# Optimization experiments

Hardware: AMD Instinct MI355X
Metric: run time of the kernel (lower is better)

Reference implementation:

```python
import jax, jax.numpy as jnp
import numpy as np

N_NODES = 50000
N_EDGES = 800000
N_GRAPHS = 128
F_IN = 128
HID = 64
EDGE_DIM = 16
H1, H2 = 4, 2
NEG_SLOPE = 0.2


def _glorot(key, shape, fan_in):
    return jax.random.normal(key, shape, dtype=jnp.float32) / np.sqrt(fan_in)


def setup_inputs() -> dict:
    key = jax.random.key(0)
    ks = jax.random.split(key, 20)
    x = jax.random.normal(ks[0], (N_NODES, F_IN), dtype=jnp.float32)
    edge_attr = jax.random.normal(ks[1], (N_EDGES, EDGE_DIM), dtype=jnp.float32)
    edge_index = jax.random.randint(ks[2], (2, N_EDGES), 0, N_NODES, dtype=jnp.int32)
    # evenly spread graph ids so every graph is non-empty (sorted)
    batch = (jnp.arange(N_NODES, dtype=jnp.int32) * N_GRAPHS) // N_NODES
    p = {
        'W1': _glorot(ks[3], (F_IN, H1 * HID), F_IN),
        'a_src1': _glorot(ks[4], (H1, HID), HID),
        'a_dst1': _glorot(ks[5], (H1, HID), HID),
        'We1': _glorot(ks[6], (EDGE_DIM, H1 * HID), EDGE_DIM),
        'a_e1': _glorot(ks[7], (H1, HID), HID),
        'b1': jnp.zeros((H1 * HID,), jnp.float32),
        'W2': _glorot(ks[8], (H1 * HID, H2 * HID), H1 * HID),
        'a_src2': _glorot(ks[9], (H2, HID), HID),
        'a_dst2': _glorot(ks[10], (H2, HID), HID),
        'We2': _glorot(ks[11], (EDGE_DIM, H2 * HID), EDGE_DIM),
        'a_e2': _glorot(ks[12], (H2, HID), HID),
        'b2': jnp.zeros((HID,), jnp.float32),
        'Wr': _glorot(ks[13], (HID, 1), HID),
        'br': jnp.zeros((1,), jnp.float32),
    }
    return dict(x=x, edge_attr=edge_attr, edge_index=edge_index, batch=batch, **p)


def _segment_softmax(scores, seg, num_segments):
    # scores: [E, H], softmax grouped by seg (destination node)
    m = jax.ops.segment_max(scores, seg, num_segments)
    m = jnp.where(jnp.isfinite(m), m, 0.0)
    ex = jnp.exp(scores - m[seg])
    s = jax.ops.segment_sum(ex, seg, num_segments)
    return ex / (s[seg] + 1e-16)


def _add_self_loops(edge_index, edge_attr, n):
    # PyG add_self_loops with fill_value='mean': per-dst mean of edge_attr
    src, dst = edge_index[0], edge_index[1]
    cnt = jax.ops.segment_sum(jnp.ones((src.shape[0],), jnp.float32), dst, n)
    loop_attr = jax.ops.segment_sum(edge_attr, dst, n) / jnp.maximum(cnt, 1.0)[:, None]
    loop = jnp.arange(n, dtype=src.dtype)
    return (jnp.concatenate([src, loop]), jnp.concatenate([dst, loop]),
            jnp.concatenate([edge_attr, loop_attr], axis=0))


def _gat_layer(x, e_attr, src, dst, W, a_src, a_dst, We, a_e, b, heads, outc, concat):
    n = x.shape[0]
    xs = (x @ W).reshape(n, heads, outc)                 # [N,H,C]
    s_src = jnp.einsum('nhc,hc->nh', xs, a_src)
    s_dst = jnp.einsum('nhc,hc->nh', xs, a_dst)
    ee = (e_attr @ We).reshape(-1, heads, outc)          # [E,H,C]
    s_e = jnp.einsum('ehc,hc->eh', ee, a_e)
    score = jax.nn.leaky_relu(s_src[src] + s_dst[dst] + s_e, NEG_SLOPE)  # [E,H]
    alpha = _segment_softmax(score, dst, n)
    out = jax.ops.segment_sum(xs[src] * alpha[..., None], dst, n)        # [N,H,C]
    out = out.reshape(n, heads * outc) if concat else out.mean(axis=1)
    return out + b


def reference(x, edge_attr, edge_index, batch,
              W1, a_src1, a_dst1, We1, a_e1, b1,
              W2, a_src2, a_dst2, We2, a_e2, b2, Wr, br):
    n = x.shape[0]
    src, dst, ea = _add_self_loops(edge_index, edge_attr, n)
    h = _gat_layer(x, ea, src, dst, W1, a_src1, a_dst1, We1, a_e1, b1, H1, HID, True)
    h = jax.nn.relu(h)
    h = _gat_layer(h, ea, src, dst, W2, a_src2, a_dst2, We2, a_e2, b2, H2, HID, False)
    g = jax.ops.segment_max(h, batch, N_GRAPHS)          # global max pool [G, HID]
    return g @ Wr + br
```

## Files before the change

### kernel.cpp

```cpp
#include <hip/hip_runtime.h>
#include <hip/hip_bf16.h>
#include <hip/hip_fp16.h>

#define DEVINL __device__ __forceinline__
typedef __hip_bfloat16 bf16;

typedef __attribute__((ext_vector_type(8))) __bf16 bf16x8;
typedef __attribute__((ext_vector_type(4))) float f32x4;

static constexpr int N_NODES  = 50000;
static constexpr int N_EDGES  = 800000;
static constexpr int N_GRAPHS = 128;
static constexpr float NEG_SLOPE = 0.2f;

DEVINL float ldIn(const void* __restrict__ p, size_t i, int isbf) {
    if (isbf) return __bfloat162float(((const bf16*)p)[i]);
    return ((const float*)p)[i];
}

DEVINL unsigned short f2bf(float f) {
    bf16 b = __float2bfloat16(f);
    return *reinterpret_cast<unsigned short*>(&b);
}

DEVINL unsigned f2hbits(float f) {
    __half h = __float2half(f);
    return (unsigned)*reinterpret_cast<unsigned short*>(&h);
}

DEVINL float hbits2f(unsigned bits) {
    unsigned short us = (unsigned short)bits;
    __half h = *reinterpret_cast<__half*>(&us);
    return __half2float(h);
}

DEVINL float lrelu_exp(float sc) {
    sc = sc > 0.f ? sc : NEG_SLOPE * sc;
    return __expf(sc);
}

DEVINL void accw(float w, unsigned wv, float& a0, float& a1) {
    a0 = fmaf(w, __uint_as_float(wv << 16), a0);
    a1 = fmaf(w, __uint_as_float(wv & 0xffff0000u), a1);
}

template<int H>
DEVINL float getse(const uint4& rv, int h) {
    unsigned bits;
    if (H == 4) {
        unsigned w16 = (h & 2) ? rv.z : rv.y;
        bits = (h & 1) ? (w16 >> 16) : (w16 & 0xffffu);
    } else {
        bits = h ? (rv.w >> 16) : (rv.w & 0xffffu);
    }
    return hbits2f(bits);
}

template<int CPL> struct XVT;
template<> struct XVT<8> { using T = uint4; };
template<> struct XVT<4> { using T = uint2; };

__global__ void detect_dtype_kernel(const unsigned short* __restrict__ xu,
                                    int* __restrict__ flag)
{
    int t = threadIdx.x;
    int bad = 0;
    for (int i = t; i < 1024; i += 64) {
        unsigned u = xu[2 * i];
        float v = __uint_as_float(u << 16);
        if (!(fabsf(v) <= 1e4f)) bad = 1;
    }
    unsigned long long m = __ballot(bad);
    if (t == 0) *flag = m ? 0 : 1;
}

__global__ void build_M_kernel(const void* __restrict__ We1, const void* __restrict__ ae1,
                               const void* __restrict__ We2, const void* __restrict__ ae2,
                               const int* __restrict__ flagp,
                               float* __restrict__ M1, float* __restrict__ M2)
{
    const int isbf = *flagp;
    int t = threadIdx.x;
    if (t < 64) {
        int d = t >> 2, h = t & 3;
        float s = 0.f;
        for (int c = 0; c < 64; ++c)
            s += ldIn(We1, d * 256 + h * 64 + c, isbf) * ldIn(ae1, h * 64 + c, isbf);
        M1[d * 4 + h] = s;
    }
    if (t < 32) {
        int d = t >> 1, h = t & 1;
        float s = 0.f;
        for (int c = 0; c < 64; ++c)
            s += ldIn(We2, d * 128 + h * 64 + c, isbf) * ldIn(ae2, h * 64 + c, isbf);
        M2[d * 2 + h] = s;
    }
}

template<int K, int M>
__global__ void build_wfrag_kernel(const void* __restrict__ W, const int* __restrict__ flagp,
                                   bf16* __restrict__ Wfrag)
{
    constexpr int KS = K / 32;
    const int isbf = *flagp;
    int idx = blockIdx.x * 256 + threadIdx.x;
    constexpr int total = (M / 16) * KS * 64 * 8;
    if (idx >= total) return;
    int j    = idx & 7;
    int lane = (idx >> 3) & 63;
    int rem  = idx >> 9;
    int ks   = rem % KS;
    int ct   = rem / KS;
    int k = ks * 32 + (lane >> 4) * 8 + j;
    int n = ct * 16 + (lane & 15);
    Wfrag[idx] = __float2bfloat16(ldIn(W, (size_t)k * M + n, isbf));
}

template<int K, int M, int AMODE, int H>
__global__ __launch_bounds__(256)
void gemm_mfma_kernel(const void* __restrict__ A, const bf16* __restrict__ Wfrag,
                      bf16* __restrict__ C, const int* __restrict__ flagp, int N,
                      const void* __restrict__ a_src, const void* __restrict__ a_dst,
                      float* __restrict__ sA, float* __restrict__ sD)
{
    constexpr int KS = K / 32, CT = M / 16;
    constexpr int LDA = K + 8;
    __shared__ __align__(16) unsigned short Asm[64 * LDA];
    const int isbf = *flagp;
    const int tid  = threadIdx.x;
    const int wave = tid >> 6, lane = tid & 63;
    const int n0 = blockIdx.x * 64;

    for (int i = tid; i < 64 * (K / 8); i += 256) {
        int r  = i / (K / 8);
        int kc = (i % (K / 8)) * 8;
        int n  = n0 + r;
        unsigned short v[8] = {0, 0, 0, 0, 0, 0, 0, 0};
        if (n < N) {
            size_t base = (size_t)n * K + kc;
            if (AMODE == 1 || isbf) {
                *reinterpret_cast<uint4*>(v) =
                    *reinterpret_cast<const uint4*>((const unsigned short*)A + base);
            } else {
                const float* Af = (const float*)A + base;
                float4 f0 = *reinterpret_cast<const float4*>(Af);
                float4 f1 = *reinterpret_cast<const float4*>(Af + 4);
                v[0] = f2bf(f0.x); v[1] = f2bf(f0.y); v[2] = f2bf(f0.z); v[3] = f2bf(f0.w);
                v[4] = f2bf(f1.x); v[5] = f2bf(f1.y); v[6] = f2bf(f1.z); v[7] = f2bf(f1.w);
            }
        }
        *reinterpret_cast<uint4*>(&Asm[r * LDA + kc]) = *reinterpret_cast<uint4*>(v);
    }
    __syncthreads();

    f32x4 acc[CT];
    #pragma unroll
    for (int ct = 0; ct < CT; ++ct) acc[ct] = (f32x4){0.f, 0.f, 0.f, 0.f};

    const int arow  = wave * 16 + (lane & 15);
    const int akoff = (lane >> 4) * 8;
    #pragma unroll
    for (int ks = 0; ks < KS; ++ks) {
        bf16x8 af = *reinterpret_cast<const bf16x8*>(&Asm[arow * LDA + ks * 32 + akoff]);
        #pragma unroll
        for (int ct = 0; ct < CT; ++ct) {
            bf16x8 bfr = *reinterpret_cast<const bf16x8*>(
                &Wfrag[(((size_t)ct * KS + ks) * 64 + lane) * 8]);
            acc[ct] = __builtin_amdgcn_mfma_f32_16x16x32_bf16(af, bfr, acc[ct], 0, 0, 0);
        }
    }

    const int crow0 = n0 + wave * 16 + (lane >> 4) * 4;
    const int ccol  = lane & 15;
    #pragma unroll
    for (int ct = 0; ct < CT; ++ct) {
        #pragma unroll
        for (int r = 0; r < 4; ++r) {
            int row = crow0 + r;
            if (row < N) C[(size_t)row * M + ct * 16 + ccol] = __float2bfloat16(acc[ct][r]);
        }
    }

    float psA[4][H], psD[4][H];
    #pragma unroll
    for (int r = 0; r < 4; ++r)
        #pragma unroll
        for (int hh = 0; hh < H; ++hh) { psA[r][hh] = 0.f; psD[r][hh] = 0.f; }
    #pragma unroll
    for (int ct = 0; ct < CT; ++ct) {
        float as = ldIn(a_src, ct * 16 + ccol, isbf);
        float ad = ldIn(a_dst, ct * 16 + ccol, isbf);
        const int hh = ct >> 2;
        #pragma unroll
        for (int r = 0; r < 4; ++r) {
            psA[r][hh] += acc[ct][r] * as;
            psD[r][hh] += acc[ct][r] * ad;
        }
    }
    #pragma unroll
    for (int m = 1; m < 16; m <<= 1) {
        #pragma unroll
        for (int r = 0; r < 4; ++r)
            #pragma unroll
            for (int hh = 0; hh < H; ++hh) {
                psA[r][hh] += __shfl_xor(psA[r][hh], m);
                psD[r][hh] += __shfl_xor(psD[r][hh], m);
            }
    }
    if (ccol == 0) {
        #pragma unroll
        for (int r = 0; r < 4; ++r) {
            int row = crow0 + r;
            if (row < N) {
                #pragma unroll
                for (int hh = 0; hh < H; ++hh) {
                    sA[(size_t)row * H + hh] = psA[r][hh];
                    sD[(size_t)row * H + hh] = psD[r][hh];
                }
            }
        }
    }
}

__global__ void csr_count_kernel(const int* __restrict__ dst, int* __restrict__ cnt,
                                 int* __restrict__ rank)
{
    int e = blockIdx.x * blockDim.x + threadIdx.x;
    if (e >= N_EDGES) return;
    rank[e] = atomicAdd(&cnt[dst[e]], 1);
}

__global__ __launch_bounds__(256)
void scan_sum_kernel(const int* __restrict__ cnt, int* __restrict__ bsum)
{
    __shared__ int sm[256];
    int i = blockIdx.x * 256 + threadIdx.x;
    sm[threadIdx.x] = (i < N_NODES) ? cnt[i] : 0;
    __syncthreads();
    for (int off = 128; off; off >>= 1) {
        if (threadIdx.x < off) sm[threadIdx.x] += sm[threadIdx.x + off];
        __syncthreads();
    }
    if (threadIdx.x == 0) bsum[blockIdx.x] = sm[0];
}

__global__ __launch_bounds__(256)
void scan_off_kernel(int* __restrict__ bsum, int nb)
{
    __shared__ int sm[256];
    int tid = threadIdx.x;
    int v = (tid < nb) ? bsum[tid] : 0;
    sm[tid] = v;
    __syncthreads();
    for (int off = 1; off < 256; off <<= 1) {
        int t = (tid >= off) ? sm[tid - off] : 0;
        __syncthreads();
        sm[tid] += t;
        __syncthreads();
    }
    if (tid < nb) bsum[tid] = sm[tid] - v;
}

__global__ __launch_bounds__(256)
void scan_final_kernel(const int* __restrict__ cnt, const int* __restrict__ bsum,
                       int* __restrict__ row)
{
    __shared__ int sm[256];
    int i = blockIdx.x * 256 + threadIdx.x;
    int tid = threadIdx.x;
    int v = (i < N_NODES) ? cnt[i] : 0;
    sm[tid] = v;
    __syncthreads();
    for (int off = 1; off < 256; off <<= 1) {
        int t = (tid >= off) ? sm[tid - off] : 0;
        __syncthreads();
        sm[tid] += t;
        __syncthreads();
    }
    int excl = sm[tid] - v + bsum[blockIdx.x];
    if (i < N_NODES) row[i] = excl;
    if (i == N_NODES - 1) row[N_NODES] = excl + v;
}

__global__ void csr_scatter_kernel(const int* __restrict__ srcI, const int* __restrict__ dstI,
                                   const void* __restrict__ eattr, const int* __restrict__ flagp,
                                   const float* __restrict__ M1, const float* __restrict__ M2,
                                   const int* __restrict__ row, const int* __restrict__ rank,
                                   uint4* __restrict__ erec)
{
    const int isbf = *flagp;
    int e = blockIdx.x * blockDim.x + threadIdx.x;
    if (e >= N_EDGES) return;
    float attr[16];
    #pragma unroll
    for (int k = 0; k < 16; ++k) attr[k] = ldIn(eattr, (size_t)e * 16 + k, isbf);
    float4 o1 = {0.f, 0.f, 0.f, 0.f};
    float2 o2 = {0.f, 0.f};
    #pragma unroll
    for (int k = 0; k < 16; ++k) {
        o1.x += attr[k] * M1[k * 4 + 0];
        o1.y += attr[k] * M1[k * 4 + 1];
        o1.z += attr[k] * M1[k * 4 + 2];
        o1.w += attr[k] * M1[k * 4 + 3];
        o2.x += attr[k] * M2[k * 2 + 0];
        o2.y += attr[k] * M2[k * 2 + 1];
    }
    int pos = row[dstI[e]] + rank[e];
    uint4 rec;
    rec.x = (unsigned)srcI[e];
    rec.y = f2hbits(o1.x) | (f2hbits(o1.y) << 16);
    rec.z = f2hbits(o1.z) | (f2hbits(o1.w) << 16);
    rec.w = f2hbits(o2.x) | (f2hbits(o2.y) << 16);
    erec[pos] = rec;
}

template<int H, int LAYER>
__global__ __launch_bounds__(256)
void agg_fused_kernel(const int* __restrict__ row, const uint4* __restrict__ erec,
                      const bf16* __restrict__ xs,
                      const float* __restrict__ sA, const float* __restrict__ sD,
                      const void* __restrict__ bias,
                      const int* __restrict__ flagp, void* __restrict__ out)
{
    constexpr int CPL = (H * 64) / 32;
    using XV = typename XVT<CPL>::T;
    const int isbf = *flagp;
    int dv = (blockIdx.x * 256 + threadIdx.x) >> 6;
    const int d = __builtin_amdgcn_readfirstlane(dv);
    const int lane = threadIdx.x & 63;
    if (d >= N_NODES) return;
    const int sub = lane >> 5;
    const int sl  = lane & 31;
    const int h = (sl * CPL) >> 6;
    const unsigned short* xsu = (const unsigned short*)xs;
    const float sDv = sD[(size_t)d * H + h];
    const float sAd = sA[(size_t)d * H + h];

    float acc[CPL];
    #pragma unroll
    for (int i = 0; i < CPL; ++i) acc[i] = 0.f;
    float den = 0.f, seSum = 0.f;

    const int b = row[d], eend = row[d + 1];
    const int nb8 = (eend - b) & ~7;

    for (int j0 = b; j0 < b + nb8; j0 += 8) {
        uint4 rv[4];
        int   s[4];
        XV    xv[4];
        float sa[4], se[4];
        #pragma unroll
        for (int u = 0; u < 4; ++u) rv[u] = erec[j0 + 2 * u + sub];
        #pragma unroll
        for (int u = 0; u < 4; ++u) s[u] = (int)rv[u].x;
        #pragma unroll
        for (int u = 0; u < 4; ++u)
            xv[u] = *reinterpret_cast<const XV*>(&xsu[(size_t)s[u] * (H * 64) + sl * CPL]);
        #pragma unroll
        for (int u = 0; u < 4; ++u) sa[u] = sA[(size_t)s[u] * H + h];
        #pragma unroll
        for (int u = 0; u < 4; ++u) se[u] = getse<H>(rv[u], h);
        #pragma unroll
        for (int u = 0; u < 4; ++u) {
            float w = lrelu_exp(sa[u] + sDv + se[u]);
            seSum += se[u];
            den += w;
            const unsigned* wv = reinterpret_cast<const unsigned*>(&xv[u]);
            #pragma unroll
            for (int p = 0; p < CPL / 2; ++p) accw(w, wv[p], acc[2 * p], acc[2 * p + 1]);
        }
    }
    for (int j0 = b + nb8; j0 < eend; j0 += 2) {
        int jj = j0 + sub;
        bool valid = jj < eend;
        int jc = valid ? jj : (eend - 1);
        uint4 rv = erec[jc];
        int s = (int)rv.x;
        float se = getse<H>(rv, h);
        float sa = sA[(size_t)s * H + h];
        XV xv = *reinterpret_cast<const XV*>(&xsu[(size_t)s * (H * 64) + sl * CPL]);
        float w = valid ? lrelu_exp(sa + sDv + se) : 0.f;
        seSum += valid ? se : 0.f;
        den += w;
        const unsigned* wv = reinterpret_cast<const unsigned*>(&xv);
        #pragma unroll
        for (int p = 0; p < CPL / 2; ++p) accw(w, wv[p], acc[2 * p], acc[2 * p + 1]);
    }

    #pragma unroll
    for (int i = 0; i < CPL; ++i) acc[i] += __shfl_xor(acc[i], 32);
    den   += __shfl_xor(den, 32);
    seSum += __shfl_xor(seSum, 32);

    {
        const int cntv = eend - b;
        const float seM = seSum / fmaxf((float)cntv, 1.f);
        const float wS = lrelu_exp(sAd + sDv + seM);
        XV xv = *reinterpret_cast<const XV*>(&xsu[(size_t)d * (H * 64) + sl * CPL]);
        den += wS;
        const unsigned* wv = reinterpret_cast<const unsigned*>(&xv);
        #pragma unroll
        for (int p = 0; p < CPL / 2; ++p) accw(wS, wv[p], acc[2 * p], acc[2 * p + 1]);
    }

    const float rden = 1.f / (den + 1e-16f);
    if (LAYER == 1) {
        if (sub == 0) {
            unsigned o[CPL / 2];
            #pragma unroll
            for (int p = 0; p < CPL / 2; ++p) {
                float v0 = acc[2 * p] * rden + ldIn(bias, sl * CPL + 2 * p, isbf);
                float v1 = acc[2 * p + 1] * rden + ldIn(bias, sl * CPL + 2 * p + 1, isbf);
                v0 = v0 > 0.f ? v0 : 0.f;
                v1 = v1 > 0.f ? v1 : 0.f;
                o[p] = (unsigned)f2bf(v0) | ((unsigned)f2bf(v1) << 16);
            }
            *reinterpret_cast<uint4*>(&((unsigned short*)out)[(size_t)d * (H * 64) + sl * CPL]) =
                *reinterpret_cast<uint4*>(o);
        }
    } else {
        float v[CPL], p[CPL];
        #pragma unroll
        for (int i = 0; i < CPL; ++i) {
            v[i] = acc[i] * rden;
            p[i] = __shfl_xor(v[i], 16);
        }
        if (lane < 16) {
            float4 o;
            o.x = 0.5f * (v[0] + p[0]) + ldIn(bias, sl * 4 + 0, isbf);
            o.y = 0.5f * (v[1] + p[1]) + ldIn(bias, sl * 4 + 1, isbf);
            o.z = 0.5f * (v[2] + p[2]) + ldIn(bias, sl * 4 + 2, isbf);
            o.w = 0.5f * (v[3] + p[3]) + ldIn(bias, sl * 4 + 3, isbf);
            *reinterpret_cast<float4*>(&((float*)out)[(size_t)d * 64 + sl * 4]) = o;
        }
    }
}

__global__ __launch_bounds__(256)
void pool_max_kernel(const float* __restrict__ h2, const int* __restrict__ batch,
                     float* __restrict__ g)
{
    int gi = blockIdx.x;
    int lo = 0, hi = N_NODES;
    while (lo < hi) { int mid = (lo + hi) >> 1; if (batch[mid] < gi) lo = mid + 1; else hi = mid; }
    int start = lo;
    lo = start; hi = N_NODES;
    while (lo < hi) { int mid = (lo + hi) >> 1; if (batch[mid] < gi + 1) lo = mid + 1; else hi = mid; }
    int end = lo;
    int c = threadIdx.x & 63, chunk = threadIdx.x >> 6;
    float m = -INFINITY;
    for (int n = start + chunk; n < end; n += 4) m = fmaxf(m, h2[(size_t)n * 64 + c]);
    __shared__ float sm[256];
    sm[threadIdx.x] = m;
    __syncthreads();
    if (threadIdx.x < 64) {
        m = fmaxf(fmaxf(sm[threadIdx.x], sm[threadIdx.x + 64]),
                  fmaxf(sm[threadIdx.x + 128], sm[threadIdx.x + 192]));
        g[gi * 64 + threadIdx.x] = m;
    }
}

__global__ void readout_kernel(const float* __restrict__ g, const void* __restrict__ Wr,
                               const void* __restrict__ br, const int* __restrict__ flagp,
                               void* __restrict__ out)
{
    const int isbf = *flagp;
    int gi = blockIdx.x;
    int lane = threadIdx.x;
    float p = g[gi * 64 + lane] * ldIn(Wr, lane, isbf);
    for (int off = 32; off; off >>= 1) p += __shfl_down(p, off);
    if (lane == 0) {
        float r = p + ldIn(br, 0, isbf);
        if (isbf) ((bf16*)out)[gi] = __float2bfloat16(r);
        else      ((float*)out)[gi] = r;
    }
}

extern "C" void kernel_launch(void* const* d_in, const int* in_sizes, int n_in,
                              void* d_out, int out_size, void* d_ws, size_t ws_size,
                              hipStream_t stream)
{
    const void* x     = d_in[0];
    const void* ea    = d_in[1];
    const int*  eidx  = (const int*)d_in[2];
    const int*  batch = (const int*)d_in[3];
    const void* W1  = d_in[4];
    const void* as1 = d_in[5];
    const void* ad1 = d_in[6];
    const void* We1 = d_in[7];
    const void* ae1 = d_in[8];
    const void* b1  = d_in[9];
    const void* W2  = d_in[10];
    const void* as2 = d_in[11];
    const void* ad2 = d_in[12];
    const void* We2 = d_in[13];
    const void* ae2 = d_in[14];
    const void* b2  = d_in[15];
    const void* Wr  = d_in[16];
    const void* br  = d_in[17];

    const int* srcI = eidx;
    const int* dstI = eidx + N_EDGES;

    float* ws    = (float*)d_ws;
    bf16*  xs    = (bf16*)ws;
    bf16*  h1    = (bf16*)(ws + 6400000);
    float* h2    = ws + 6400000;
    uint4* erec  = (uint4*)(ws + 12800000);
    float* sA1   = ws + 16000000;
    float* sD1   = ws + 16200000;
    float* sA2   = ws + 16400000;
    float* sD2   = ws + 16500000;
    int*   ib    = (int*)(ws + 16600000);
    int*   row    = ib;
    int*   cnt    = ib + 50016;
    int*   bsum   = ib + 100032;
    int*   rank   = ib + 100384;
    float* misc  = ws + 16600000 + 900384;
    int*   flag  = (int*)misc;
    float* M1    = misc + 16;
    float* M2    = misc + 80;
    float* gpool = misc + 112;
    bf16*  wf1   = (bf16*)(misc + 8320);
    bf16*  wf2   = (bf16*)(misc + 8320 + 16384);

    hipMemsetAsync(cnt, 0, N_NODES * sizeof(int), stream);

    detect_dtype_kernel<<<1, 64, 0, stream>>>((const unsigned short*)x, flag);
    build_M_kernel<<<1, 64, 0, stream>>>(We1, ae1, We2, ae2, flag, M1, M2);
    build_wfrag_kernel<128, 256><<<128, 256, 0, stream>>>(W1, flag, wf1);
    build_wfrag_kernel<256, 128><<<128, 256, 0, stream>>>(W2, flag, wf2);

    const int NB = (N_NODES + 255) / 256;
    csr_count_kernel<<<(N_EDGES + 255) / 256, 256, 0, stream>>>(dstI, cnt, rank);
    scan_sum_kernel<<<NB, 256, 0, stream>>>(cnt, bsum);
    scan_off_kernel<<<1, 256, 0, stream>>>(bsum, NB);
    scan_final_kernel<<<NB, 256, 0, stream>>>(cnt, bsum, row);
    csr_scatter_kernel<<<(N_EDGES + 255) / 256, 256, 0, stream>>>(
        srcI, dstI, ea, flag, M1, M2, row, rank, erec);

    const int GB = (N_NODES + 63) / 64;

    gemm_mfma_kernel<128, 256, 0, 4><<<GB, 256, 0, stream>>>(
        x, wf1, xs, flag, N_NODES, as1, ad1, sA1, sD1);
    agg_fused_kernel<4, 1><<<(N_NODES + 3) / 4, 256, 0, stream>>>(
        row, erec, xs, sA1, sD1, b1, flag, h1);

    gemm_mfma_kernel<256, 128, 1, 2><<<GB, 256, 0, stream>>>(
        h1, wf2, xs, flag, N_NODES, as2, ad2, sA2, sD2);
    agg_fused_kernel<2, 2><<<(N_NODES + 3) / 4, 256, 0, stream>>>(
        row, erec, xs, sA2, sD2, b2, flag, h2);

    pool_max_kernel<<<N_GRAPHS, 256, 0, stream>>>(h2, batch, gpool);
    readout_kernel<<<N_GRAPHS, 64, 0, stream>>>(gpool, Wr, br, flag, d_out);
}
```

Before: 423.9 us.

## Process four edges per wave in aggregation and fuse prep and pool/readout kernels

The aggregation kernel now splits each 64-lane wave into four 16-lane groups, each handling a different edge with wider 16-byte gathers per lane, in place of two 32-lane halves. A second xor-shuffle stage combines the partial sums. The three weight-prep kernels are merged into one launch, and max-pool is fused with the readout. The aim is more memory-level parallelism in the gather-bound aggregation and fewer small launches, at the cost of more registers per lane and an extra reduction step.

Result: faster. 411.3 us (-3.0%).

```diff
diff --git a/kernel.cpp b/kernel.cpp
--- a/kernel.cpp
+++ b/kernel.cpp
@@ -56,10 +56,6 @@
     return hbits2f(bits);
 }
 
-template<int CPL> struct XVT;
-template<> struct XVT<8> { using T = uint4; };
-template<> struct XVT<4> { using T = uint2; };
-
 __global__ void detect_dtype_kernel(const unsigned short* __restrict__ xu,
                                     int* __restrict__ flag)
 {
@@ -74,36 +70,11 @@
     if (t == 0) *flag = m ? 0 : 1;
 }
 
-__global__ void build_M_kernel(const void* __restrict__ We1, const void* __restrict__ ae1,
-                               const void* __restrict__ We2, const void* __restrict__ ae2,
-                               const int* __restrict__ flagp,
-                               float* __restrict__ M1, float* __restrict__ M2)
-{
-    const int isbf = *flagp;
-    int t = threadIdx.x;
-    if (t < 64) {
-        int d = t >> 2, h = t & 3;
-        float s = 0.f;
-        for (int c = 0; c < 64; ++c)
-            s += ldIn(We1, d * 256 + h * 64 + c, isbf) * ldIn(ae1, h * 64 + c, isbf);
-        M1[d * 4 + h] = s;
-    }
-    if (t < 32) {
-        int d = t >> 1, h = t & 1;
-        float s = 0.f;
-        for (int c = 0; c < 64; ++c)
-            s += ldIn(We2, d * 128 + h * 64 + c, isbf) * ldIn(ae2, h * 64 + c, isbf);
-        M2[d * 2 + h] = s;
-    }
-}
-
 template<int K, int M>
-__global__ void build_wfrag_kernel(const void* __restrict__ W, const int* __restrict__ flagp,
-                                   bf16* __restrict__ Wfrag)
+DEVINL void wfrag_build(const void* __restrict__ W, int isbf,
+                        bf16* __restrict__ Wfrag, int idx)
 {
     constexpr int KS = K / 32;
-    const int isbf = *flagp;
-    int idx = blockIdx.x * 256 + threadIdx.x;
     constexpr int total = (M / 16) * KS * 64 * 8;
     if (idx >= total) return;
     int j    = idx & 7;
@@ -114,6 +85,39 @@
     int k = ks * 32 + (lane >> 4) * 8 + j;
     int n = ct * 16 + (lane & 15);
     Wfrag[idx] = __float2bfloat16(ldIn(W, (size_t)k * M + n, isbf));
+}
+
+__global__ __launch_bounds__(256)
+void prep_kernel(const void* __restrict__ We1, const void* __restrict__ ae1,
+                 const void* __restrict__ We2, const void* __restrict__ ae2,
+                 const void* __restrict__ W1,  const void* __restrict__ W2,
+                 const int* __restrict__ flagp,
+                 float* __restrict__ M1, float* __restrict__ M2,
+                 bf16* __restrict__ wf1, bf16* __restrict__ wf2)
+{
+    const int isbf = *flagp;
+    const int bx = blockIdx.x;
+    const int t  = threadIdx.x;
+    if (bx == 0) {
+        if (t < 64) {
+            int d = t >> 2, h = t & 3;
+            float s = 0.f;
+            for (int c = 0; c < 64; ++c)
+                s += ldIn(We1, d * 256 + h * 64 + c, isbf) * ldIn(ae1, h * 64 + c, isbf);
+            M1[d * 4 + h] = s;
+        }
+        if (t < 32) {
+            int d = t >> 1, h = t & 1;
+            float s = 0.f;
+            for (int c = 0; c < 64; ++c)
+                s += ldIn(We2, d * 128 + h * 64 + c, isbf) * ldIn(ae2, h * 64 + c, isbf);
+            M2[d * 2 + h] = s;
+        }
+    } else if (bx <= 128) {
+        wfrag_build<128, 256>(W1, isbf, wf1, (bx - 1) * 256 + t);
+    } else {
+        wfrag_build<256, 128>(W2, isbf, wf2, (bx - 129) * 256 + t);
+    }
 }
 
 template<int K, int M, int AMODE, int H>
@@ -322,17 +326,19 @@
                       const void* __restrict__ bias,
                       const int* __restrict__ flagp, void* __restrict__ out)
 {
-    constexpr int CPL = (H * 64) / 32;
-    using XV = typename XVT<CPL>::T;
+    constexpr int C   = H * 64;
+    constexpr int CPL = C / 16;
+    constexpr int NQ  = CPL / 8;
     const int isbf = *flagp;
     int dv = (blockIdx.x * 256 + threadIdx.x) >> 6;
     const int d = __builtin_amdgcn_readfirstlane(dv);
     const int lane = threadIdx.x & 63;
     if (d >= N_NODES) return;
-    const int sub = lane >> 5;
-    const int sl  = lane & 31;
-    const int h = (sl * CPL) >> 6;
-    const unsigned short* xsu = (const unsigned short*)xs;
+    const int q  = lane >> 4;
+    const int sl = lane & 15;
+    const int h  = (sl * CPL) >> 6;
+    const char* xsb = (const char*)xs;
+    const unsigned lb = (unsigned)(sl * (CPL * 2));
     const float sDv = sD[(size_t)d * H + h];
     const float sAd = sA[(size_t)d * H + h];
 
@@ -342,70 +348,78 @@
     float den = 0.f, seSum = 0.f;
 
     const int b = row[d], eend = row[d + 1];
-    const int nb8 = (eend - b) & ~7;
+    const int cnt = eend - b;
+    const int nb8 = cnt & ~7;
 
     for (int j0 = b; j0 < b + nb8; j0 += 8) {
-        uint4 rv[4];
-        int   s[4];
-        XV    xv[4];
-        float sa[4], se[4];
-        #pragma unroll
-        for (int u = 0; u < 4; ++u) rv[u] = erec[j0 + 2 * u + sub];
-        #pragma unroll
-        for (int u = 0; u < 4; ++u) s[u] = (int)rv[u].x;
-        #pragma unroll
-        for (int u = 0; u < 4; ++u)
-            xv[u] = *reinterpret_cast<const XV*>(&xsu[(size_t)s[u] * (H * 64) + sl * CPL]);
-        #pragma unroll
-        for (int u = 0; u < 4; ++u) sa[u] = sA[(size_t)s[u] * H + h];
-        #pragma unroll
-        for (int u = 0; u < 4; ++u) se[u] = getse<H>(rv[u], h);
-        #pragma unroll
-        for (int u = 0; u < 4; ++u) {
-            float w = lrelu_exp(sa[u] + sDv + se[u]);
-            seSum += se[u];
-            den += w;
-            const unsigned* wv = reinterpret_cast<const unsigned*>(&xv[u]);
-            #pragma unroll
-            for (int p = 0; p < CPL / 2; ++p) accw(w, wv[p], acc[2 * p], acc[2 * p + 1]);
-        }
-    }
-    for (int j0 = b + nb8; j0 < eend; j0 += 2) {
-        int jj = j0 + sub;
+        uint4 rv0 = erec[j0 + q];
+        uint4 rv1 = erec[j0 + 4 + q];
+        int s0 = (int)rv0.x, s1 = (int)rv1.x;
+        const uint4* p0 = (const uint4*)(xsb + (size_t)((unsigned)s0 * (C * 2) + lb));
+        const uint4* p1 = (const uint4*)(xsb + (size_t)((unsigned)s1 * (C * 2) + lb));
+        uint4 xv0[NQ], xv1[NQ];
+        #pragma unroll
+        for (int t = 0; t < NQ; ++t) { xv0[t] = p0[t]; xv1[t] = p1[t]; }
+        float sa0 = sA[(size_t)s0 * H + h];
+        float sa1 = sA[(size_t)s1 * H + h];
+        float se0 = getse<H>(rv0, h);
+        float se1 = getse<H>(rv1, h);
+        float w0 = lrelu_exp(sa0 + sDv + se0);
+        float w1 = lrelu_exp(sa1 + sDv + se1);
+        seSum += se0 + se1;
+        den += w0 + w1;
+        const unsigned* wv0 = reinterpret_cast<const unsigned*>(xv0);
+        const unsigned* wv1 = reinterpret_cast<const unsigned*>(xv1);
+        #pragma unroll
+        for (int p = 0; p < CPL / 2; ++p) {
+            accw(w0, wv0[p], acc[2 * p], acc[2 * p + 1]);
+            accw(w1, wv1[p], acc[2 * p], acc[2 * p + 1]);
+        }
+    }
+    for (int j0 = b + nb8; j0 < eend; j0 += 4) {
+        int jj = j0 + q;
         bool valid = jj < eend;
         int jc = valid ? jj : (eend - 1);
         uint4 rv = erec[jc];
         int s = (int)rv.x;
+        const uint4* p0 = (const uint4*)(xsb + (size_t)((unsigned)s * (C * 2) + lb));
+        uint4 xv[NQ];
+        #pragma unroll
+        for (int t = 0; t < NQ; ++t) xv[t] = p0[t];
+        float sa = sA[(size_t)s * H + h];
         float se = getse<H>(rv, h);
-        float sa = sA[(size_t)s * H + h];
-        XV xv = *reinterpret_cast<const XV*>(&xsu[(size_t)s * (H * 64) + sl * CPL]);
         float w = valid ? lrelu_exp(sa + sDv + se) : 0.f;
         seSum += valid ? se : 0.f;
         den += w;
-        const unsigned* wv = reinterpret_cast<const unsigned*>(&xv);
+        const unsigned* wv = reinterpret_cast<const unsigned*>(xv);
         #pragma unroll
         for (int p = 0; p < CPL / 2; ++p) accw(w, wv[p], acc[2 * p], acc[2 * p + 1]);
     }
 
     #pragma unroll
-    for (int i = 0; i < CPL; ++i) acc[i] += __shfl_xor(acc[i], 32);
-    den   += __shfl_xor(den, 32);
-    seSum += __shfl_xor(seSum, 32);
+    for (int i = 0; i < CPL; ++i) {
+        acc[i] += __shfl_xor(acc[i], 16);
+        acc[i] += __shfl_xor(acc[i], 32);
+    }
+    den   += __shfl_xor(den, 16);   den   += __shfl_xor(den, 32);
+    seSum += __shfl_xor(seSum, 16); seSum += __shfl_xor(seSum, 32);
 
     {
-        const int cntv = eend - b;
-        const float seM = seSum / fmaxf((float)cntv, 1.f);
-        const float wS = lrelu_exp(sAd + sDv + seM);
-        XV xv = *reinterpret_cast<const XV*>(&xsu[(size_t)d * (H * 64) + sl * CPL]);
+        const float seM = seSum / fmaxf((float)cnt, 1.f);
+        const float wS  = lrelu_exp(sAd + sDv + seM);
+        const uint4* p0 = (const uint4*)(xsb + (size_t)((unsigned)d * (C * 2) + lb));
+        uint4 xvS[NQ];
+        #pragma unroll
+        for (int t = 0; t < NQ; ++t) xvS[t] = p0[t];
         den += wS;
-        const unsigned* wv = reinterpret_cast<const unsigned*>(&xv);
+        const unsigned* wv = reinterpret_cast<const unsigned*>(xvS);
         #pragma unroll
         for (int p = 0; p < CPL / 2; ++p) accw(wS, wv[p], acc[2 * p], acc[2 * p + 1]);
     }
 
     const float rden = 1.f / (den + 1e-16f);
     if (LAYER == 1) {
-        if (sub == 0) {
+        if (q == 0) {
             unsigned o[CPL / 2];
             #pragma unroll
             for (int p = 0; p < CPL / 2; ++p) {
@@ -415,31 +429,36 @@
                 v1 = v1 > 0.f ? v1 : 0.f;
                 o[p] = (unsigned)f2bf(v0) | ((unsigned)f2bf(v1) << 16);
             }
-            *reinterpret_cast<uint4*>(&((unsigned short*)out)[(size_t)d * (H * 64) + sl * CPL]) =
-                *reinterpret_cast<uint4*>(o);
+            uint4* op = reinterpret_cast<uint4*>(
+                &((unsigned short*)out)[(size_t)d * C + sl * CPL]);
+            op[0] = reinterpret_cast<uint4*>(o)[0];
+            if (NQ == 2) op[1] = reinterpret_cast<uint4*>(o)[1];
         }
     } else {
-        float v[CPL], p[CPL];
+        float v[CPL], pp[CPL];
         #pragma unroll
         for (int i = 0; i < CPL; ++i) {
             v[i] = acc[i] * rden;
-            p[i] = __shfl_xor(v[i], 16);
-        }
-        if (lane < 16) {
-            float4 o;
-            o.x = 0.5f * (v[0] + p[0]) + ldIn(bias, sl * 4 + 0, isbf);
-            o.y = 0.5f * (v[1] + p[1]) + ldIn(bias, sl * 4 + 1, isbf);
-            o.z = 0.5f * (v[2] + p[2]) + ldIn(bias, sl * 4 + 2, isbf);
-            o.w = 0.5f * (v[3] + p[3]) + ldIn(bias, sl * 4 + 3, isbf);
-            *reinterpret_cast<float4*>(&((float*)out)[(size_t)d * 64 + sl * 4]) = o;
-        }
-    }
-}
-
-__global__ __launch_bounds__(256)
-void pool_max_kernel(const float* __restrict__ h2, const int* __restrict__ batch,
-                     float* __restrict__ g)
-{
+            pp[i] = __shfl_xor(v[i], 8);
+        }
+        if (q == 0 && sl < 8) {
+            float o[CPL];
+            #pragma unroll
+            for (int i = 0; i < CPL; ++i)
+                o[i] = 0.5f * (v[i] + pp[i]) + ldIn(bias, sl * CPL + i, isbf);
+            float4* op = reinterpret_cast<float4*>(&((float*)out)[(size_t)d * 64 + sl * CPL]);
+            op[0] = reinterpret_cast<float4*>(o)[0];
+            op[1] = reinterpret_cast<float4*>(o)[1];
+        }
+    }
+}
+
+__global__ __launch_bounds__(256)
+void pool_readout_kernel(const float* __restrict__ h2, const int* __restrict__ batch,
+                         const void* __restrict__ Wr, const void* __restrict__ br,
+                         const int* __restrict__ flagp, void* __restrict__ out)
+{
+    const int isbf = *flagp;
     int gi = blockIdx.x;
     int lo = 0, hi = N_NODES;
     while (lo < hi) { int mid = (lo + hi) >> 1; if (batch[mid] < gi) lo = mid + 1; else hi = mid; }
@@ -456,23 +475,13 @@
     if (threadIdx.x < 64) {
         m = fmaxf(fmaxf(sm[threadIdx.x], sm[threadIdx.x + 64]),
                   fmaxf(sm[threadIdx.x + 128], sm[threadIdx.x + 192]));
-        g[gi * 64 + threadIdx.x] = m;
-    }
-}
-
-__global__ void readout_kernel(const float* __restrict__ g, const void* __restrict__ Wr,
-                               const void* __restrict__ br, const int* __restrict__ flagp,
-                               void* __restrict__ out)
-{
-    const int isbf = *flagp;
-    int gi = blockIdx.x;
-    int lane = threadIdx.x;
-    float p = g[gi * 64 + lane] * ldIn(Wr, lane, isbf);
-    for (int off = 32; off; off >>= 1) p += __shfl_down(p, off);
-    if (lane == 0) {
-        float r = p + ldIn(br, 0, isbf);
-        if (isbf) ((bf16*)out)[gi] = __float2bfloat16(r);
-        else      ((float*)out)[gi] = r;
+        float p = m * ldIn(Wr, threadIdx.x, isbf);
+        for (int off = 32; off; off >>= 1) p += __shfl_down(p, off);
+        if (threadIdx.x == 0) {
+            float r = p + ldIn(br, 0, isbf);
+            if (isbf) ((bf16*)out)[gi] = __float2bfloat16(r);
+            else      ((float*)out)[gi] = r;
+        }
     }
 }
 
@@ -520,16 +529,14 @@
     int*   flag  = (int*)misc;
     float* M1    = misc + 16;
     float* M2    = misc + 80;
-    float* gpool = misc + 112;
     bf16*  wf1   = (bf16*)(misc + 8320);
     bf16*  wf2   = (bf16*)(misc + 8320 + 16384);
 
     hipMemsetAsync(cnt, 0, N_NODES * sizeof(int), stream);
 
     detect_dtype_kernel<<<1, 64, 0, stream>>>((const unsigned short*)x, flag);
-    build_M_kernel<<<1, 64, 0, stream>>>(We1, ae1, We2, ae2, flag, M1, M2);
-    build_wfrag_kernel<128, 256><<<128, 256, 0, stream>>>(W1, flag, wf1);
-    build_wfrag_kernel<256, 128><<<128, 256, 0, stream>>>(W2, flag, wf2);
+    prep_kernel<<<257, 256, 0, stream>>>(We1, ae1, We2, ae2, W1, W2, flag,
+                                         M1, M2, wf1, wf2);
 
     const int NB = (N_NODES + 255) / 256;
     csr_count_kernel<<<(N_EDGES + 255) / 256, 256, 0, stream>>>(dstI, cnt, rank);
@@ -551,6 +558,5 @@
     agg_fused_kernel<2, 2><<<(N_NODES + 3) / 4, 256, 0, stream>>>(
         row, erec, xs, sA2, sD2, b2, flag, h2);
 
-    pool_max_kernel<<<N_GRAPHS, 256, 0, stream>>>(h2, batch, gpool);
-    readout_kernel<<<N_GRAPHS, 64, 0, stream>>>(gpool, Wr, br, flag, d_out);
-}
+    pool_readout_kernel<<<N_GRAPHS, 256, 0, stream>>>(h2, batch, Wr, br, flag, d_out);
+}
```
